# Kernel optimization log

Hardware: AMD Instinct MI355X
Metric: run time of the kernel (lower is better)

## Reference

```python
import jax, jax.numpy as jnp
import numpy as np

B, L, D = 1, 2048, 512
NL, N, K = 4, 16, 4
DI = 2 * D          # mamba expand=2
R = D // 16         # dt_rank = ceil(D/16)
H = 4 * D           # mlp hidden


def _ln(x, w, b, eps=1e-5):
    mu = x.mean(-1, keepdims=True)
    v = ((x - mu) ** 2).mean(-1, keepdims=True)
    return (x - mu) * jax.lax.rsqrt(v + eps) * w + b


def _rms(x, w, eps=1e-5):
    return x * jax.lax.rsqrt((x * x).mean(-1, keepdims=True) + eps) * w


def _ssm_scan(delta, Bm, Cm, u, A, Dp):
    # delta,u: (B,L,DI); Bm,Cm: (B,L,N); A: (DI,N); Dp: (DI,)
    def step(h, inp):
        d_t, b_t, c_t, u_t = inp                              # (B,DI),(B,N),(B,N),(B,DI)
        dA = jnp.exp(d_t[..., None] * A)                      # (B,DI,N)
        h = dA * h + (d_t * u_t)[..., None] * b_t[:, None, :]
        y = jnp.einsum('bdn,bn->bd', h, c_t)
        return h, y
    h0 = jnp.zeros((delta.shape[0], DI, N), delta.dtype)
    xs = (delta.swapaxes(0, 1), Bm.swapaxes(0, 1), Cm.swapaxes(0, 1), u.swapaxes(0, 1))
    _, ys = jax.lax.scan(step, h0, xs)
    return ys.swapaxes(0, 1) + u * Dp


def _mamba(h, in_w, cw, cb, xw, dtw, dtb, A_log, Dp, ow):
    xz = h @ in_w.T                                           # (B,L,2*DI)
    x, z = jnp.split(xz, 2, axis=-1)
    # causal depthwise conv1d, kernel K, left pad K-1
    xp = jnp.pad(x, ((0, 0), (K - 1, 0), (0, 0)))
    Ls = x.shape[1]
    x = sum(cw[:, k] * xp[:, k:k + Ls, :] for k in range(K)) + cb
    x = jax.nn.silu(x)
    dbc = x @ xw.T                                            # (B,L,R+2N)
    dt, Bm, Cm = dbc[..., :R], dbc[..., R:R + N], dbc[..., R + N:]
    delta = jax.nn.softplus(dt @ dtw.T + dtb)                 # (B,L,DI)
    A = -jnp.exp(A_log)                                       # (DI,N)
    y = _ssm_scan(delta, Bm, Cm, x, A, Dp)
    y = y * jax.nn.silu(z)
    return y @ ow.T


def _forward(hidden_states, ln1_w, ln1_b, in_proj_w, conv_w, conv_b, x_proj_w,
             dt_proj_w, dt_proj_b, A_log, D_param, out_proj_w, block_norm_w,
             norm_f_w, ln2_w, ln2_b, fc1_w, fc1_b, fc2_w, fc2_b):
    shortcut = hidden_states
    h = _ln(hidden_states, ln1_w, ln1_b)
    residual = None
    for i in range(in_proj_w.shape[0]):
        residual = h if residual is None else h + residual    # residual_in_fp32
        hn = _rms(residual, block_norm_w[i])                  # fused_add_norm prenorm
        h = _mamba(hn, in_proj_w[i], conv_w[i], conv_b[i], x_proj_w[i],
                   dt_proj_w[i], dt_proj_b[i], A_log[i], D_param[i], out_proj_w[i])
    h = _rms(h + residual, norm_f_w)                          # final rms_norm_fn
    h = shortcut + h
    x = _ln(h, ln2_w, ln2_b)
    x = jax.nn.gelu(x @ fc1_w.T + fc1_b)
    x = x @ fc2_w.T + fc2_b
    return h + x


def setup_inputs() -> dict:
    key = jax.random.key(0)
    ks = jax.random.split(key, 9)
    s = 0.02
    return {
        'hidden_states': jax.random.normal(ks[0], (B, L, D), jnp.float32),
        'ln1_w': jnp.ones((D,), jnp.float32),
        'ln1_b': jnp.zeros((D,), jnp.float32),
        'in_proj_w': jax.random.normal(ks[1], (NL, 2 * DI, D), jnp.float32) * s,
        'conv_w': jax.random.normal(ks[2], (NL, DI, K), jnp.float32) * 0.3,
        'conv_b': jnp.zeros((NL, DI), jnp.float32),
        'x_proj_w': jax.random.normal(ks[3], (NL, R + 2 * N, DI), jnp.float32) * s,
        'dt_proj_w': jax.random.normal(ks[4], (NL, DI, R), jnp.float32) * s,
        'dt_proj_b': jax.random.uniform(ks[5], (NL, DI), jnp.float32, -4.0, -2.0),
        'A_log': jnp.tile(jnp.log(jnp.arange(1, N + 1, dtype=jnp.float32)), (NL, DI, 1)),
        'D_param': jnp.ones((NL, DI), jnp.float32),
        'out_proj_w': jax.random.normal(ks[6], (NL, D, DI), jnp.float32) * s,
        'block_norm_w': jnp.ones((NL, D), jnp.float32),
        'norm_f_w': jnp.ones((D,), jnp.float32),
        'ln2_w': jnp.ones((D,), jnp.float32),
        'ln2_b': jnp.zeros((D,), jnp.float32),
        'fc1_w': jax.random.normal(ks[7], (H, D), jnp.float32) * s,
        'fc1_b': jnp.zeros((H,), jnp.float32),
        'fc2_w': jax.random.normal(ks[8], (D, H), jnp.float32) * s,
        'fc2_b': jnp.zeros((D,), jnp.float32),
    }


def reference(hidden_states, ln1_w, ln1_b, in_proj_w, conv_w, conv_b, x_proj_w,
              dt_proj_w, dt_proj_b, A_log, D_param, out_proj_w, block_norm_w,
              norm_f_w, ln2_w, ln2_b, fc1_w, fc1_b, fc2_w, fc2_b):
    return _forward(hidden_states, ln1_w, ln1_b, in_proj_w, conv_w, conv_b,
                    x_proj_w, dt_proj_w, dt_proj_b, A_log, D_param, out_proj_w,
                    block_norm_w, norm_f_w, ln2_w, ln2_b, fc1_w, fc1_b, fc2_w, fc2_b)
```

## Files before the change

kernel.cpp:

```cpp
#include <hip/hip_runtime.h>
#include <hip/hip_bf16.h>
#include <math.h>

#define L_SEQ 2048
#define Dm    512
#define DI    1024
#define Nst   16
#define Kc    4
#define Rr    32
#define NL    4
#define CH    128
#define LC    (L_SEQ / CH)

typedef __attribute__((ext_vector_type(8))) short bf16x8;
typedef __attribute__((ext_vector_type(4))) float f32x4;

__device__ __forceinline__ float act_softplus(float x) {
    return fmaxf(x, 0.f) + log1pf(__expf(-fabsf(x)));
}
__device__ __forceinline__ float act_gelu(float x) {
    float c = 0.7978845608028654f * (x + 0.044715f * x * x * x);
    float t = 1.f - 2.f / (__expf(2.f * c) + 1.f);
    return 0.5f * x * (1.f + t);
}
__device__ __forceinline__ float silu_(float x) {
    return x / (1.f + __expf(-x));
}
__device__ __forceinline__ ushort f2bf(float f) {
    union { float f; unsigned u; } c; c.f = f;
    unsigned r = c.u + 0x7fffu + ((c.u >> 16) & 1u);
    return (ushort)(r >> 16);
}
__device__ __forceinline__ float bf2f(ushort u) {
    union { unsigned u; float f; } c; c.u = ((unsigned)u) << 16;
    return c.f;
}

__global__ __launch_bounds__(256) void cast_all_kernel(
    const float* __restrict__ s0, ushort* __restrict__ d0, int n0,
    const float* __restrict__ s1, ushort* __restrict__ d1, int n1,
    const float* __restrict__ s2, ushort* __restrict__ d2, int n2,
    const float* __restrict__ s3, ushort* __restrict__ d3, int n3,
    const float* __restrict__ s4, ushort* __restrict__ d4, int n4_,
    const float* __restrict__ s5, ushort* __restrict__ d5, int n5)
{
    int i = blockIdx.x * 256 + threadIdx.x;
    const float* s; ushort* d;
    if (i < n0) { s = s0; d = d0; }
    else { i -= n0; if (i < n1) { s = s1; d = d1; }
    else { i -= n1; if (i < n2) { s = s2; d = d2; }
    else { i -= n2; if (i < n3) { s = s3; d = d3; }
    else { i -= n3; if (i < n4_) { s = s4; d = d4; }
    else { i -= n4_; if (i < n5) { s = s5; d = d5; } else return; } } } } }
    float4 v = ((const float4*)s)[i];
    ushort4 o;
    o.x = f2bf(v.x); o.y = f2bf(v.y); o.z = f2bf(v.z); o.w = f2bf(v.w);
    ((ushort4*)d)[i] = o;
}

__global__ __launch_bounds__(256) void ln_kernel(const float* __restrict__ x,
    const float* __restrict__ w, const float* __restrict__ b, float* __restrict__ y)
{
    int row = blockIdx.x;
    int i0 = threadIdx.x, i1 = threadIdx.x + 256;
    const float* xr = x + (size_t)row * Dm;
    float v0 = xr[i0], v1 = xr[i1];
    float s = v0 + v1, ss = v0 * v0 + v1 * v1;
    for (int off = 32; off; off >>= 1) { s += __shfl_down(s, off); ss += __shfl_down(ss, off); }
    __shared__ float red[10];
    int wid = threadIdx.x >> 6;
    if ((threadIdx.x & 63) == 0) { red[wid] = s; red[4 + wid] = ss; }
    __syncthreads();
    if (threadIdx.x == 0) {
        float S = red[0] + red[1] + red[2] + red[3];
        float SS = red[4] + red[5] + red[6] + red[7];
        float mu = S * (1.f / Dm);
        float var = SS * (1.f / Dm) - mu * mu;
        red[8] = mu; red[9] = rsqrtf(var + 1e-5f);
    }
    __syncthreads();
    float mu = red[8], rs = red[9];
    y[(size_t)row * Dm + i0] = (v0 - mu) * rs * w[i0] + b[i0];
    y[(size_t)row * Dm + i1] = (v1 - mu) * rs * w[i1] + b[i1];
}

__global__ __launch_bounds__(256) void add_rms_kernel(const float* __restrict__ a,
    const float* __restrict__ bsrc, float* __restrict__ sum_out,
    const float* __restrict__ w, ushort* __restrict__ rms_out)
{
    int row = blockIdx.x;
    int i0 = threadIdx.x, i1 = threadIdx.x + 256;
    size_t base = (size_t)row * Dm;
    float v0 = a[base + i0], v1 = a[base + i1];
    if (bsrc) { v0 += bsrc[base + i0]; v1 += bsrc[base + i1]; }
    sum_out[base + i0] = v0; sum_out[base + i1] = v1;
    float ss = v0 * v0 + v1 * v1;
    for (int off = 32; off; off >>= 1) ss += __shfl_down(ss, off);
    __shared__ float red[5];
    if ((threadIdx.x & 63) == 0) red[threadIdx.x >> 6] = ss;
    __syncthreads();
    if (threadIdx.x == 0) red[4] = rsqrtf((red[0] + red[1] + red[2] + red[3]) * (1.f / Dm) + 1e-5f);
    __syncthreads();
    float rs = red[4];
    rms_out[base + i0] = f2bf(v0 * rs * w[i0]);
    rms_out[base + i1] = f2bf(v1 * rs * w[i1]);
}

__global__ __launch_bounds__(256) void final_ln2_kernel(const float* __restrict__ h,
    const float* __restrict__ res, const float* __restrict__ shortcut,
    const float* __restrict__ wf, const float* __restrict__ w2,
    const float* __restrict__ b2, float* __restrict__ hout,
    ushort* __restrict__ yb16)
{
    int row = blockIdx.x;
    int i0 = threadIdx.x, i1 = threadIdx.x + 256;
    size_t base = (size_t)row * Dm;
    float v0 = h[base + i0] + res[base + i0];
    float v1 = h[base + i1] + res[base + i1];
    float ss = v0 * v0 + v1 * v1;
    for (int off = 32; off; off >>= 1) ss += __shfl_down(ss, off);
    __shared__ float red[10];
    if ((threadIdx.x & 63) == 0) red[threadIdx.x >> 6] = ss;
    __syncthreads();
    if (threadIdx.x == 0) red[4] = rsqrtf((red[0] + red[1] + red[2] + red[3]) * (1.f / Dm) + 1e-5f);
    __syncthreads();
    float rs = red[4];
    float t0 = shortcut[base + i0] + v0 * rs * wf[i0];
    float t1 = shortcut[base + i1] + v1 * rs * wf[i1];
    hout[base + i0] = t0;
    hout[base + i1] = t1;
    __syncthreads();
    float s = t0 + t1, ss2 = t0 * t0 + t1 * t1;
    for (int off = 32; off; off >>= 1) { s += __shfl_down(s, off); ss2 += __shfl_down(ss2, off); }
    int wid = threadIdx.x >> 6;
    if ((threadIdx.x & 63) == 0) { red[wid] = s; red[5 + wid] = ss2; }
    __syncthreads();
    if (threadIdx.x == 0) {
        float S = red[0] + red[1] + red[2] + red[3];
        float SS = red[5] + red[6] + red[7] + red[8];
        float mu = S * (1.f / Dm);
        float var = SS * (1.f / Dm) - mu * mu;
        red[4] = mu; red[9] = rsqrtf(var + 1e-5f);
    }
    __syncthreads();
    float mu = red[4], rsig = red[9];
    yb16[base + i0] = f2bf((t0 - mu) * rsig * w2[i0] + b2[i0]);
    yb16[base + i1] = f2bf((t1 - mu) * rsig * w2[i1] + b2[i1]);
}

template<int BM, int BN, int BK, int EPI, int KS = 1>
__global__ __launch_bounds__(256) void gemm_mfma(
    const ushort* __restrict__ A, int lda,
    const ushort* __restrict__ W, int K,
    void* __restrict__ Cout, int ldc,
    const float* __restrict__ bias, const float* __restrict__ addsrc,
    size_t split_stride)
{
    constexpr int ROWB  = BK * 2;
    constexpr int SMASK = (ROWB / 16) - 1;
    constexpr int KK    = BK / 32;
    constexpr int WM = BM / 2, WN = BN / 2;
    constexpr int FM = WM / 16, FN = WN / 16;
    constexpr int ISS_A = (BM * ROWB) / 4096;
    constexpr int ISS_W = (BN * ROWB) / 4096;

    __shared__ __align__(16) ushort As[BM * BK];
    __shared__ __align__(16) ushort Ws[BN * BK];

    int tid = threadIdx.x;
    int wave = tid >> 6, lane = tid & 63;
    int wr = wave >> 1, wc = wave & 1;
    int l16 = lane & 15, lk = lane >> 4;
    int bm = blockIdx.y * BM, bn = blockIdx.x * BN;

    int kbeg = 0, kend = K;
    float* coutf = (float*)Cout;
    if constexpr (KS > 1) {
        int Kper = K / KS;
        kbeg = blockIdx.z * Kper; kend = kbeg + Kper;
        coutf += split_stride * blockIdx.z;
    }

    const ushort* srcA[ISS_A];
    const ushort* srcW[ISS_W];
    #pragma unroll
    for (int s = 0; s < ISS_A; ++s) {
        int off = s * 4096 + wave * 1024 + lane * 16;
        int row = off / ROWB;
        int slot = (off % ROWB) >> 4;
        int col = ((slot ^ (row & SMASK)) << 3);
        srcA[s] = A + (size_t)(bm + row) * lda + col;
    }
    #pragma unroll
    for (int s = 0; s < ISS_W; ++s) {
        int off = s * 4096 + wave * 1024 + lane * 16;
        int row = off / ROWB;
        int slot = (off % ROWB) >> 4;
        int col = ((slot ^ (row & SMASK)) << 3);
        srcW[s] = W + (size_t)(bn + row) * K + col;
    }
    int aoff[FM][KK], woff[FN][KK];
    #pragma unroll
    for (int i = 0; i < FM; ++i) {
        int row = wr * WM + i * 16 + l16;
        #pragma unroll
        for (int kk = 0; kk < KK; ++kk)
            aoff[i][kk] = row * BK + ((((kk << 2) | lk) ^ (row & SMASK)) << 3);
    }
    #pragma unroll
    for (int j = 0; j < FN; ++j) {
        int row = wc * WN + j * 16 + l16;
        #pragma unroll
        for (int kk = 0; kk < KK; ++kk)
            woff[j][kk] = row * BK + ((((kk << 2) | lk) ^ (row & SMASK)) << 3);
    }

    f32x4 acc[FM][FN] = {};

    for (int k0 = kbeg; k0 < kend; k0 += BK) {
        #pragma unroll
        for (int s = 0; s < ISS_A; ++s)
            __builtin_amdgcn_global_load_lds(
                (const __attribute__((address_space(1))) void*)(srcA[s] + k0),
                (__attribute__((address_space(3))) void*)((char*)As + s * 4096 + wave * 1024),
                16, 0, 0);
        #pragma unroll
        for (int s = 0; s < ISS_W; ++s)
            __builtin_amdgcn_global_load_lds(
                (const __attribute__((address_space(1))) void*)(srcW[s] + k0),
                (__attribute__((address_space(3))) void*)((char*)Ws + s * 4096 + wave * 1024),
                16, 0, 0);
        __syncthreads();
        #pragma unroll
        for (int kk = 0; kk < KK; ++kk) {
            bf16x8 af[FM], wf[FN];
            #pragma unroll
            for (int i = 0; i < FM; ++i) af[i] = *(const bf16x8*)(As + aoff[i][kk]);
            #pragma unroll
            for (int j = 0; j < FN; ++j) wf[j] = *(const bf16x8*)(Ws + woff[j][kk]);
            #pragma unroll
            for (int i = 0; i < FM; ++i)
                #pragma unroll
                for (int j = 0; j < FN; ++j)
                    acc[i][j] = __builtin_amdgcn_mfma_f32_16x16x32_bf16(af[i], wf[j], acc[i][j], 0, 0, 0);
        }
        __syncthreads();
    }

    int orow0 = bm + wr * WM, ocol0 = bn + wc * WN;
    #pragma unroll
    for (int j = 0; j < FN; ++j) {
        int col = ocol0 + j * 16 + l16;
        float bj = 0.f;
        if constexpr (EPI == 2 || EPI == 4) bj = bias[col];
        #pragma unroll
        for (int i = 0; i < FM; ++i) {
            #pragma unroll
            for (int r = 0; r < 4; ++r) {
                int row = orow0 + i * 16 + lk * 4 + r;
                float v = acc[i][j][r];
                if constexpr (EPI == 0) {
                    coutf[(size_t)row * ldc + col] = v;
                } else if constexpr (EPI == 1) {
                    ((ushort*)Cout)[(size_t)row * ldc + col] = f2bf(v);
                } else if constexpr (EPI == 2) {
                    ((ushort*)Cout)[(size_t)row * ldc + col] = f2bf(act_gelu(v + bj));
                } else if constexpr (EPI == 4) {
                    ((float*)Cout)[(size_t)row * ldc + col] = v + bj + addsrc[(size_t)row * ldc + col];
                }
            }
        }
    }
}

__global__ __launch_bounds__(256) void xfin_kernel(
    const float* __restrict__ part, const ushort* __restrict__ wdt,
    const float* __restrict__ dtb, float* __restrict__ dbc,
    ushort* __restrict__ delta_bf)
{
    __shared__ float sdt[8][32];
    int tid = threadIdx.x;
    int t0 = blockIdx.x * 8;
    const int S = L_SEQ * 64;
    #pragma unroll
    for (int i = tid; i < 512; i += 256) {
        int tt = i >> 6, c = i & 63;
        int idx = (t0 + tt) * 64 + c;
        float s = part[idx] + part[idx + S] + part[idx + 2 * S] + part[idx + 3 * S];
        if (c < 32) sdt[tt][c] = s;
        else dbc[idx] = s;
    }
    __syncthreads();
    int d0 = tid * 4;
    bf16x8 w[4][4];
    float b4[4];
    #pragma unroll
    for (int q = 0; q < 4; ++q) {
        b4[q] = dtb[d0 + q];
        #pragma unroll
        for (int p = 0; p < 4; ++p)
            w[q][p] = *(const bf16x8*)(wdt + (size_t)(d0 + q) * 32 + p * 8);
    }
    for (int tt = 0; tt < 8; ++tt) {
        float acc[4] = { b4[0], b4[1], b4[2], b4[3] };
        #pragma unroll
        for (int p = 0; p < 4; ++p)
            #pragma unroll
            for (int e = 0; e < 8; ++e) {
                float sv = sdt[tt][p * 8 + e];
                #pragma unroll
                for (int q = 0; q < 4; ++q)
                    acc[q] = fmaf(sv, bf2f((ushort)w[q][p][e]), acc[q]);
            }
        ushort4 o;
        o.x = f2bf(act_softplus(acc[0]));
        o.y = f2bf(act_softplus(acc[1]));
        o.z = f2bf(act_softplus(acc[2]));
        o.w = f2bf(act_softplus(acc[3]));
        *(ushort4*)(delta_bf + (size_t)(t0 + tt) * DI + d0) = o;
    }
}

__global__ __launch_bounds__(256) void conv_silu_kernel(const ushort* __restrict__ xz,
    const float* __restrict__ cw, const float* __restrict__ cb, ushort* __restrict__ xc)
{
    int g = blockIdx.x * 256 + threadIdx.x;
    int e = g * 8;
    int d0 = e & (DI - 1);
    int t = e >> 10;
    float acc[8];
    #pragma unroll
    for (int q = 0; q < 8; ++q) acc[q] = cb[d0 + q];
    float4 cwv[8];
    #pragma unroll
    for (int q = 0; q < 8; ++q) cwv[q] = *(const float4*)(cw + (size_t)(d0 + q) * 4);
    #pragma unroll
    for (int k = 0; k < 4; ++k) {
        int tt = t + k - 3;
        if (tt >= 0) {
            bf16x8 xv = *(const bf16x8*)(xz + (size_t)tt * (2 * DI) + d0);
            #pragma unroll
            for (int q = 0; q < 8; ++q) {
                float wk = (k == 0) ? cwv[q].x : (k == 1) ? cwv[q].y : (k == 2) ? cwv[q].z : cwv[q].w;
                acc[q] = fmaf(wk, bf2f((ushort)xv[q]), acc[q]);
            }
        }
    }
    bf16x8 o;
    #pragma unroll
    for (int q = 0; q < 8; ++q) o[q] = (short)f2bf(silu_(acc[q]));
    *(bf16x8*)(xc + e) = o;
}

__global__ __launch_bounds__(256) void scan_chunk_kernel(
    const ushort* __restrict__ delta, const ushort* __restrict__ u,
    const float* __restrict__ dbc, const float* __restrict__ A_log,
    float* __restrict__ hend, float* __restrict__ aprod)
{
    __shared__ float bs[LC][16];
    int tid = threadIdx.x;
    int c = blockIdx.x;
    int d = blockIdx.y * 256 + tid;
    int t0 = c * LC;
    {
        int tt = tid >> 4, nn = tid & 15;
        bs[tt][nn] = dbc[(size_t)(t0 + tt) * 64 + 32 + nn];
    }
    float A2[16];
    {
        float a[16];
        #pragma unroll
        for (int q = 0; q < 4; ++q)
            *(float4*)(a + q * 4) = ((const float4*)(A_log + (size_t)d * 16))[q];
        #pragma unroll
        for (int n = 0; n < 16; ++n)
            A2[n] = -__expf(a[n]) * 1.44269504f;
    }
    float h[16], ap[16];
    #pragma unroll
    for (int n = 0; n < 16; ++n) { h[n] = 0.f; ap[n] = 1.f; }
    __syncthreads();
    for (int tt = 0; tt < LC; ++tt) {
        int t = t0 + tt;
        float dt_ = bf2f(delta[(size_t)t * DI + d]);
        float du = dt_ * bf2f(u[(size_t)t * DI + d]);
        #pragma unroll
        for (int n = 0; n < 16; ++n) {
            float dA = exp2f(dt_ * A2[n]);
            h[n] = fmaf(dA, h[n], du * bs[tt][n]);
            ap[n] *= dA;
        }
    }
    size_t base = ((size_t)c * DI + d) * 16;
    #pragma unroll
    for (int q = 0; q < 4; ++q) {
        ((float4*)(hend + base))[q]  = *(float4*)(h + q * 4);
        ((float4*)(aprod + base))[q] = *(float4*)(ap + q * 4);
    }
}

__global__ __launch_bounds__(64) void chunk_prefix_kernel(
    const float* __restrict__ hend, float* __restrict__ aprod_hin)
{
    int j = blockIdx.x * 64 + threadIdx.x;
    float h = 0.f;
    for (int cg = 0; cg < CH; cg += 8) {
        float ap[8], he[8];
        #pragma unroll
        for (int q = 0; q < 8; ++q) {
            size_t o = (size_t)(cg + q) * (DI * Nst) + j;
            ap[q] = aprod_hin[o]; he[q] = hend[o];
        }
        #pragma unroll
        for (int q = 0; q < 8; ++q) {
            size_t o = (size_t)(cg + q) * (DI * Nst) + j;
            aprod_hin[o] = h;
            h = fmaf(ap[q], h, he[q]);
        }
    }
}

__global__ __launch_bounds__(256) void scan_apply_kernel(
    const ushort* __restrict__ delta, const ushort* __restrict__ u,
    const float* __restrict__ dbc, const float* __restrict__ A_log,
    const float* __restrict__ Dp, const ushort* __restrict__ xz,
    const float* __restrict__ hin, ushort* __restrict__ y)
{
    __shared__ float bs[LC][16], cs[LC][16];
    int tid = threadIdx.x;
    int c = blockIdx.x;
    int d = blockIdx.y * 256 + tid;
    int t0 = c * LC;
    #pragma unroll
    for (int i = tid; i < LC * 32; i += 256) {
        int tt = i >> 5, k = i & 31;
        float v = dbc[(size_t)(t0 + tt) * 64 + 32 + k];
        if (k < 16) bs[tt][k] = v; else cs[tt][k - 16] = v;
    }
    float A2[16];
    {
        float a[16];
        #pragma unroll
        for (int q = 0; q < 4; ++q)
            *(float4*)(a + q * 4) = ((const float4*)(A_log + (size_t)d * 16))[q];
        #pragma unroll
        for (int n = 0; n < 16; ++n)
            A2[n] = -__expf(a[n]) * 1.44269504f;
    }
    float h[16];
    size_t base = ((size_t)c * DI + d) * 16;
    #pragma unroll
    for (int q = 0; q < 4; ++q)
        *(float4*)(h + q * 4) = ((const float4*)(hin + base))[q];
    float Dval = Dp[d];
    __syncthreads();
    for (int tt = 0; tt < LC; ++tt) {
        int t = t0 + tt;
        float dt_ = bf2f(delta[(size_t)t * DI + d]);
        float u_  = bf2f(u[(size_t)t * DI + d]);
        float du  = dt_ * u_;
        float acc = 0.f;
        #pragma unroll
        for (int n = 0; n < 16; ++n) {
            float dA = exp2f(dt_ * A2[n]);
            h[n] = fmaf(dA, h[n], du * bs[tt][n]);
            acc = fmaf(h[n], cs[tt][n], acc);
        }
        float z = bf2f(xz[(size_t)t * (2 * DI) + DI + d]);
        y[(size_t)t * DI + d] = f2bf((acc + u_ * Dval) * silu_(z));
    }
}

extern "C" void kernel_launch(void* const* d_in, const int* in_sizes, int n_in,
                              void* d_out, int out_size, void* d_ws, size_t ws_size,
                              hipStream_t stream)
{
    const float* hidden     = (const float*)d_in[0];
    const float* ln1_w      = (const float*)d_in[1];
    const float* ln1_b      = (const float*)d_in[2];
    const float* in_proj_w  = (const float*)d_in[3];
    const float* conv_w     = (const float*)d_in[4];
    const float* conv_b     = (const float*)d_in[5];
    const float* x_proj_w   = (const float*)d_in[6];
    const float* dt_proj_w  = (const float*)d_in[7];
    const float* dt_proj_b  = (const float*)d_in[8];
    const float* A_log      = (const float*)d_in[9];
    const float* D_param    = (const float*)d_in[10];
    const float* out_proj_w = (const float*)d_in[11];
    const float* block_norm_w = (const float*)d_in[12];
    const float* norm_f_w   = (const float*)d_in[13];
    const float* ln2_w      = (const float*)d_in[14];
    const float* ln2_b      = (const float*)d_in[15];
    const float* fc1_w      = (const float*)d_in[16];
    const float* fc1_b      = (const float*)d_in[17];
    const float* fc2_w      = (const float*)d_in[18];
    const float* fc2_b      = (const float*)d_in[19];

    char* P = (char*)d_ws;
    auto alloc = [&](size_t bytes) { char* r = P; P += (bytes + 255) & ~(size_t)255; return r; };
    float* h      = (float*)alloc((size_t)L_SEQ * Dm * 4);
    float* hout   = (float*)alloc((size_t)L_SEQ * Dm * 4);
    float* res    = (float*)alloc((size_t)L_SEQ * Dm * 4);
    float* dbc    = (float*)alloc((size_t)L_SEQ * 64 * 4);
    float* part   = (float*)alloc((size_t)4 * L_SEQ * 64 * 4);
    float* aprod  = (float*)alloc((size_t)CH * DI * Nst * 4);
    ushort* delta_bf = (ushort*)alloc((size_t)L_SEQ * DI * 2);
    ushort* hn_bf = (ushort*)alloc((size_t)L_SEQ * Dm * 2);
    ushort* xz_bf = (ushort*)alloc((size_t)L_SEQ * 2 * DI * 2);
    ushort* xc_bf = (ushort*)alloc((size_t)L_SEQ * DI * 2);
    ushort* yb_bf = (ushort*)alloc((size_t)L_SEQ * DI * 2);
    ushort* w_in  = (ushort*)alloc((size_t)NL * 2 * DI * Dm * 2);
    ushort* w_out = (ushort*)alloc((size_t)NL * Dm * DI * 2);
    ushort* w_x   = (ushort*)alloc((size_t)NL * 64 * DI * 2);
    ushort* w_dt  = (ushort*)alloc((size_t)NL * DI * Rr * 2);
    ushort* w_fc1 = (ushort*)alloc((size_t)(4 * Dm) * Dm * 2);
    ushort* w_fc2 = (ushort*)alloc((size_t)Dm * (4 * Dm) * 2);
    float* hend = h;
    float* out  = (float*)d_out;

    {
        int n0 = NL * 2 * DI * Dm / 4, n1 = NL * Dm * DI / 4, n2 = NL * 64 * DI / 4;
        int n3 = NL * DI * Rr / 4, n4_ = 4 * Dm * Dm / 4, n5 = Dm * 4 * Dm / 4;
        int tot = n0 + n1 + n2 + n3 + n4_ + n5;
        cast_all_kernel<<<(tot + 255) / 256, 256, 0, stream>>>(
            in_proj_w, w_in, n0, out_proj_w, w_out, n1, x_proj_w, w_x, n2,
            dt_proj_w, w_dt, n3, fc1_w, w_fc1, n4_, fc2_w, w_fc2, n5);
    }

    ln_kernel<<<L_SEQ, 256, 0, stream>>>(hidden, ln1_w, ln1_b, h);

    dim3 gscan(CH, DI / 256);
    for (int i = 0; i < NL; ++i) {
        add_rms_kernel<<<L_SEQ, 256, 0, stream>>>(h, i ? res : nullptr, res,
                                                  block_norm_w + i * Dm, hn_bf);
        gemm_mfma<128, 128, 128, 1><<<dim3(2 * DI / 128, L_SEQ / 128), 256, 0, stream>>>(
            hn_bf, Dm, w_in + (size_t)i * 2 * DI * Dm, Dm, xz_bf, 2 * DI, nullptr, nullptr, 0);
        conv_silu_kernel<<<(L_SEQ * DI / 8) / 256, 256, 0, stream>>>(
            xz_bf, conv_w + i * DI * Kc, conv_b + i * DI, xc_bf);
        gemm_mfma<64, 64, 64, 0, 4><<<dim3(1, L_SEQ / 64, 4), 256, 0, stream>>>(
            xc_bf, DI, w_x + (size_t)i * 64 * DI, DI, part, 64, nullptr, nullptr,
            (size_t)L_SEQ * 64);
        xfin_kernel<<<L_SEQ / 8, 256, 0, stream>>>(part, w_dt + (size_t)i * DI * Rr,
                                        dt_proj_b + i * DI, dbc, delta_bf);
        scan_chunk_kernel<<<gscan, 256, 0, stream>>>(delta_bf, xc_bf, dbc,
                                        A_log + (size_t)i * DI * Nst, hend, aprod);
        chunk_prefix_kernel<<<(DI * Nst) / 64, 64, 0, stream>>>(hend, aprod);
        scan_apply_kernel<<<gscan, 256, 0, stream>>>(delta_bf, xc_bf, dbc,
                                        A_log + (size_t)i * DI * Nst,
                                        D_param + i * DI, xz_bf, aprod, yb_bf);
        gemm_mfma<64, 64, 128, 0><<<dim3(Dm / 64, L_SEQ / 64), 256, 0, stream>>>(
            yb_bf, DI, w_out + (size_t)i * Dm * DI, DI, h, Dm, nullptr, nullptr, 0);
    }

    final_ln2_kernel<<<L_SEQ, 256, 0, stream>>>(h, res, hidden, norm_f_w,
                                                ln2_w, ln2_b, hout, hn_bf);
    gemm_mfma<128, 128, 128, 2><<<dim3(2048 / 128, L_SEQ / 128), 256, 0, stream>>>(
        hn_bf, Dm, w_fc1, Dm, xz_bf, 2048, fc1_b, nullptr, 0);
    gemm_mfma<64, 64, 128, 4><<<dim3(Dm / 64, L_SEQ / 64), 256, 0, stream>>>(
        xz_bf, 2048, w_fc2, 2048, out, Dm, fc2_b, hout, 0);
}
```

Baseline: 456.9 us.

## Fuse LN with first RMS, use wave-per-row norms and bf16 mixer output

Merges the initial layernorm and the first block's residual/RMS norm into one kernel, which drops one launch and one full-row round trip. All row-norm kernels now process one row per wavefront with vectorized 8-element loads and shuffle reductions instead of shared-memory block reductions. The out_proj GEMM now writes bf16 instead of fp32, which halves that write and the following read but lowers the precision of the mixer output added to the residual. The scan's hend buffer gets its own allocation because the fp32 h buffer no longer exists.

Result: faster. 445.4 us (-2.5%).

```diff
diff --git a/kernel.cpp b/kernel.cpp
--- a/kernel.cpp
+++ b/kernel.cpp
@@ -34,6 +34,11 @@
 __device__ __forceinline__ float bf2f(ushort u) {
     union { unsigned u; float f; } c; c.u = ((unsigned)u) << 16;
     return c.f;
+}
+__device__ __forceinline__ float wave_sum(float v) {
+    #pragma unroll
+    for (int off = 32; off; off >>= 1) v += __shfl_xor(v, off);
+    return v;
 }
 
 __global__ __launch_bounds__(256) void cast_all_kernel(
@@ -58,94 +63,121 @@
     ((ushort4*)d)[i] = o;
 }
 
-__global__ __launch_bounds__(256) void ln_kernel(const float* __restrict__ x,
-    const float* __restrict__ w, const float* __restrict__ b, float* __restrict__ y)
-{
-    int row = blockIdx.x;
-    int i0 = threadIdx.x, i1 = threadIdx.x + 256;
-    const float* xr = x + (size_t)row * Dm;
-    float v0 = xr[i0], v1 = xr[i1];
-    float s = v0 + v1, ss = v0 * v0 + v1 * v1;
-    for (int off = 32; off; off >>= 1) { s += __shfl_down(s, off); ss += __shfl_down(ss, off); }
-    __shared__ float red[10];
-    int wid = threadIdx.x >> 6;
-    if ((threadIdx.x & 63) == 0) { red[wid] = s; red[4 + wid] = ss; }
-    __syncthreads();
-    if (threadIdx.x == 0) {
-        float S = red[0] + red[1] + red[2] + red[3];
-        float SS = red[4] + red[5] + red[6] + red[7];
-        float mu = S * (1.f / Dm);
-        float var = SS * (1.f / Dm) - mu * mu;
-        red[8] = mu; red[9] = rsqrtf(var + 1e-5f);
-    }
-    __syncthreads();
-    float mu = red[8], rs = red[9];
-    y[(size_t)row * Dm + i0] = (v0 - mu) * rs * w[i0] + b[i0];
-    y[(size_t)row * Dm + i1] = (v1 - mu) * rs * w[i1] + b[i1];
-}
-
-__global__ __launch_bounds__(256) void add_rms_kernel(const float* __restrict__ a,
-    const float* __restrict__ bsrc, float* __restrict__ sum_out,
-    const float* __restrict__ w, ushort* __restrict__ rms_out)
-{
-    int row = blockIdx.x;
-    int i0 = threadIdx.x, i1 = threadIdx.x + 256;
-    size_t base = (size_t)row * Dm;
-    float v0 = a[base + i0], v1 = a[base + i1];
-    if (bsrc) { v0 += bsrc[base + i0]; v1 += bsrc[base + i1]; }
-    sum_out[base + i0] = v0; sum_out[base + i1] = v1;
-    float ss = v0 * v0 + v1 * v1;
-    for (int off = 32; off; off >>= 1) ss += __shfl_down(ss, off);
-    __shared__ float red[5];
-    if ((threadIdx.x & 63) == 0) red[threadIdx.x >> 6] = ss;
-    __syncthreads();
-    if (threadIdx.x == 0) red[4] = rsqrtf((red[0] + red[1] + red[2] + red[3]) * (1.f / Dm) + 1e-5f);
-    __syncthreads();
-    float rs = red[4];
-    rms_out[base + i0] = f2bf(v0 * rs * w[i0]);
-    rms_out[base + i1] = f2bf(v1 * rs * w[i1]);
-}
-
-__global__ __launch_bounds__(256) void final_ln2_kernel(const float* __restrict__ h,
+__global__ __launch_bounds__(256) void ln_rms_kernel(const float* __restrict__ x,
+    const float* __restrict__ w, const float* __restrict__ b,
+    const float* __restrict__ rw, float* __restrict__ res,
+    ushort* __restrict__ hn_bf)
+{
+    int lane = threadIdx.x & 63, wv = threadIdx.x >> 6;
+    int row = blockIdx.x * 4 + wv;
+    size_t base = (size_t)row * Dm + lane * 8;
+    float v[8];
+    *(float4*)(v)     = *(const float4*)(x + base);
+    *(float4*)(v + 4) = *(const float4*)(x + base + 4);
+    float s = 0.f, ss = 0.f;
+    #pragma unroll
+    for (int q = 0; q < 8; ++q) { s += v[q]; ss += v[q] * v[q]; }
+    s = wave_sum(s); ss = wave_sum(ss);
+    float mu = s * (1.f / Dm);
+    float rs = rsqrtf(ss * (1.f / Dm) - mu * mu + 1e-5f);
+    float wv8[8], bv8[8], rv8[8];
+    *(float4*)(wv8)     = *(const float4*)(w + lane * 8);
+    *(float4*)(wv8 + 4) = *(const float4*)(w + lane * 8 + 4);
+    *(float4*)(bv8)     = *(const float4*)(b + lane * 8);
+    *(float4*)(bv8 + 4) = *(const float4*)(b + lane * 8 + 4);
+    *(float4*)(rv8)     = *(const float4*)(rw + lane * 8);
+    *(float4*)(rv8 + 4) = *(const float4*)(rw + lane * 8 + 4);
+    float o[8], ss2 = 0.f;
+    #pragma unroll
+    for (int q = 0; q < 8; ++q) {
+        o[q] = (v[q] - mu) * rs * wv8[q] + bv8[q];
+        ss2 += o[q] * o[q];
+    }
+    *(float4*)(res + base)     = *(float4*)(o);
+    *(float4*)(res + base + 4) = *(float4*)(o + 4);
+    ss2 = wave_sum(ss2);
+    float rr = rsqrtf(ss2 * (1.f / Dm) + 1e-5f);
+    bf16x8 hb;
+    #pragma unroll
+    for (int q = 0; q < 8; ++q) hb[q] = (short)f2bf(o[q] * rr * rv8[q]);
+    *(bf16x8*)(hn_bf + base) = hb;
+}
+
+__global__ __launch_bounds__(256) void add_rms_kernel(const ushort* __restrict__ hb,
+    float* __restrict__ res, const float* __restrict__ w, ushort* __restrict__ rms_out)
+{
+    int lane = threadIdx.x & 63, wv = threadIdx.x >> 6;
+    int row = blockIdx.x * 4 + wv;
+    size_t base = (size_t)row * Dm + lane * 8;
+    bf16x8 hv = *(const bf16x8*)(hb + base);
+    float v[8];
+    *(float4*)(v)     = *(const float4*)(res + base);
+    *(float4*)(v + 4) = *(const float4*)(res + base + 4);
+    float ss = 0.f;
+    #pragma unroll
+    for (int q = 0; q < 8; ++q) {
+        v[q] += bf2f((ushort)hv[q]);
+        ss += v[q] * v[q];
+    }
+    *(float4*)(res + base)     = *(float4*)(v);
+    *(float4*)(res + base + 4) = *(float4*)(v + 4);
+    ss = wave_sum(ss);
+    float rr = rsqrtf(ss * (1.f / Dm) + 1e-5f);
+    float wv8[8];
+    *(float4*)(wv8)     = *(const float4*)(w + lane * 8);
+    *(float4*)(wv8 + 4) = *(const float4*)(w + lane * 8 + 4);
+    bf16x8 ob;
+    #pragma unroll
+    for (int q = 0; q < 8; ++q) ob[q] = (short)f2bf(v[q] * rr * wv8[q]);
+    *(bf16x8*)(rms_out + base) = ob;
+}
+
+__global__ __launch_bounds__(256) void final_ln2_kernel(const ushort* __restrict__ hb,
     const float* __restrict__ res, const float* __restrict__ shortcut,
     const float* __restrict__ wf, const float* __restrict__ w2,
     const float* __restrict__ b2, float* __restrict__ hout,
     ushort* __restrict__ yb16)
 {
-    int row = blockIdx.x;
-    int i0 = threadIdx.x, i1 = threadIdx.x + 256;
-    size_t base = (size_t)row * Dm;
-    float v0 = h[base + i0] + res[base + i0];
-    float v1 = h[base + i1] + res[base + i1];
-    float ss = v0 * v0 + v1 * v1;
-    for (int off = 32; off; off >>= 1) ss += __shfl_down(ss, off);
-    __shared__ float red[10];
-    if ((threadIdx.x & 63) == 0) red[threadIdx.x >> 6] = ss;
-    __syncthreads();
-    if (threadIdx.x == 0) red[4] = rsqrtf((red[0] + red[1] + red[2] + red[3]) * (1.f / Dm) + 1e-5f);
-    __syncthreads();
-    float rs = red[4];
-    float t0 = shortcut[base + i0] + v0 * rs * wf[i0];
-    float t1 = shortcut[base + i1] + v1 * rs * wf[i1];
-    hout[base + i0] = t0;
-    hout[base + i1] = t1;
-    __syncthreads();
-    float s = t0 + t1, ss2 = t0 * t0 + t1 * t1;
-    for (int off = 32; off; off >>= 1) { s += __shfl_down(s, off); ss2 += __shfl_down(ss2, off); }
-    int wid = threadIdx.x >> 6;
-    if ((threadIdx.x & 63) == 0) { red[wid] = s; red[5 + wid] = ss2; }
-    __syncthreads();
-    if (threadIdx.x == 0) {
-        float S = red[0] + red[1] + red[2] + red[3];
-        float SS = red[5] + red[6] + red[7] + red[8];
-        float mu = S * (1.f / Dm);
-        float var = SS * (1.f / Dm) - mu * mu;
-        red[4] = mu; red[9] = rsqrtf(var + 1e-5f);
-    }
-    __syncthreads();
-    float mu = red[4], rsig = red[9];
-    yb16[base + i0] = f2bf((t0 - mu) * rsig * w2[i0] + b2[i0]);
-    yb16[base + i1] = f2bf((t1 - mu) * rsig * w2[i1] + b2[i1]);
+    int lane = threadIdx.x & 63, wv = threadIdx.x >> 6;
+    int row = blockIdx.x * 4 + wv;
+    size_t base = (size_t)row * Dm + lane * 8;
+    bf16x8 hv = *(const bf16x8*)(hb + base);
+    float v[8];
+    *(float4*)(v)     = *(const float4*)(res + base);
+    *(float4*)(v + 4) = *(const float4*)(res + base + 4);
+    float ss = 0.f;
+    #pragma unroll
+    for (int q = 0; q < 8; ++q) {
+        v[q] += bf2f((ushort)hv[q]);
+        ss += v[q] * v[q];
+    }
+    ss = wave_sum(ss);
+    float rs = rsqrtf(ss * (1.f / Dm) + 1e-5f);
+    float sc[8], wf8[8];
+    *(float4*)(sc)     = *(const float4*)(shortcut + base);
+    *(float4*)(sc + 4) = *(const float4*)(shortcut + base + 4);
+    *(float4*)(wf8)     = *(const float4*)(wf + lane * 8);
+    *(float4*)(wf8 + 4) = *(const float4*)(wf + lane * 8 + 4);
+    float t[8], s2 = 0.f, ss2 = 0.f;
+    #pragma unroll
+    for (int q = 0; q < 8; ++q) {
+        t[q] = sc[q] + v[q] * rs * wf8[q];
+        s2 += t[q]; ss2 += t[q] * t[q];
+    }
+    *(float4*)(hout + base)     = *(float4*)(t);
+    *(float4*)(hout + base + 4) = *(float4*)(t + 4);
+    s2 = wave_sum(s2); ss2 = wave_sum(ss2);
+    float mu = s2 * (1.f / Dm);
+    float rsig = rsqrtf(ss2 * (1.f / Dm) - mu * mu + 1e-5f);
+    float w28[8], b28[8];
+    *(float4*)(w28)     = *(const float4*)(w2 + lane * 8);
+    *(float4*)(w28 + 4) = *(const float4*)(w2 + lane * 8 + 4);
+    *(float4*)(b28)     = *(const float4*)(b2 + lane * 8);
+    *(float4*)(b28 + 4) = *(const float4*)(b2 + lane * 8 + 4);
+    bf16x8 ob;
+    #pragma unroll
+    for (int q = 0; q < 8; ++q) ob[q] = (short)f2bf((t[q] - mu) * rsig * w28[q] + b28[q]);
+    *(bf16x8*)(yb16 + base) = ob;
 }
 
 template<int BM, int BN, int BK, int EPI, int KS = 1>
@@ -498,12 +530,13 @@
 
     char* P = (char*)d_ws;
     auto alloc = [&](size_t bytes) { char* r = P; P += (bytes + 255) & ~(size_t)255; return r; };
-    float* h      = (float*)alloc((size_t)L_SEQ * Dm * 4);
     float* hout   = (float*)alloc((size_t)L_SEQ * Dm * 4);
     float* res    = (float*)alloc((size_t)L_SEQ * Dm * 4);
     float* dbc    = (float*)alloc((size_t)L_SEQ * 64 * 4);
     float* part   = (float*)alloc((size_t)4 * L_SEQ * 64 * 4);
+    float* hend   = (float*)alloc((size_t)CH * DI * Nst * 4);
     float* aprod  = (float*)alloc((size_t)CH * DI * Nst * 4);
+    ushort* h_bf  = (ushort*)alloc((size_t)L_SEQ * Dm * 2);
     ushort* delta_bf = (ushort*)alloc((size_t)L_SEQ * DI * 2);
     ushort* hn_bf = (ushort*)alloc((size_t)L_SEQ * Dm * 2);
     ushort* xz_bf = (ushort*)alloc((size_t)L_SEQ * 2 * DI * 2);
@@ -515,7 +548,6 @@
     ushort* w_dt  = (ushort*)alloc((size_t)NL * DI * Rr * 2);
     ushort* w_fc1 = (ushort*)alloc((size_t)(4 * Dm) * Dm * 2);
     ushort* w_fc2 = (ushort*)alloc((size_t)Dm * (4 * Dm) * 2);
-    float* hend = h;
     float* out  = (float*)d_out;
 
     {
@@ -527,11 +559,12 @@
             dt_proj_w, w_dt, n3, fc1_w, w_fc1, n4_, fc2_w, w_fc2, n5);
     }
 
-    ln_kernel<<<L_SEQ, 256, 0, stream>>>(hidden, ln1_w, ln1_b, h);
+    ln_rms_kernel<<<L_SEQ / 4, 256, 0, stream>>>(hidden, ln1_w, ln1_b,
+                                                 block_norm_w, res, hn_bf);
 
     dim3 gscan(CH, DI / 256);
     for (int i = 0; i < NL; ++i) {
-        add_rms_kernel<<<L_SEQ, 256, 0, stream>>>(h, i ? res : nullptr, res,
+        if (i) add_rms_kernel<<<L_SEQ / 4, 256, 0, stream>>>(h_bf, res,
                                                   block_norm_w + i * Dm, hn_bf);
         gemm_mfma<128, 128, 128, 1><<<dim3(2 * DI / 128, L_SEQ / 128), 256, 0, stream>>>(
             hn_bf, Dm, w_in + (size_t)i * 2 * DI * Dm, Dm, xz_bf, 2 * DI, nullptr, nullptr, 0);
@@ -548,11 +581,11 @@
         scan_apply_kernel<<<gscan, 256, 0, stream>>>(delta_bf, xc_bf, dbc,
                                         A_log + (size_t)i * DI * Nst,
                                         D_param + i * DI, xz_bf, aprod, yb_bf);
-        gemm_mfma<64, 64, 128, 0><<<dim3(Dm / 64, L_SEQ / 64), 256, 0, stream>>>(
-            yb_bf, DI, w_out + (size_t)i * Dm * DI, DI, h, Dm, nullptr, nullptr, 0);
-    }
-
-    final_ln2_kernel<<<L_SEQ, 256, 0, stream>>>(h, res, hidden, norm_f_w,
+        gemm_mfma<64, 64, 128, 1><<<dim3(Dm / 64, L_SEQ / 64), 256, 0, stream>>>(
+            yb_bf, DI, w_out + (size_t)i * Dm * DI, DI, h_bf, Dm, nullptr, nullptr, 0);
+    }
+
+    final_ln2_kernel<<<L_SEQ / 4, 256, 0, stream>>>(h_bf, res, hidden, norm_f_w,
                                                 ln2_w, ln2_b, hout, hn_bf);
     gemm_mfma<128, 128, 128, 2><<<dim3(2048 / 128, L_SEQ / 128), 256, 0, stream>>>(
         hn_bf, Dm, w_fc1, Dm, xz_bf, 2048, fc1_b, nullptr, 0);
```
